# Performance work log

Hardware: AMD Instinct MI355X
Metric: run time of the kernel (lower is better)

## Reference

```python
import jax, jax.numpy as jnp
import numpy as np

B, S, H, NH = 1, 4096, 1024, 16
DH = H // NH


def setup_inputs() -> dict:
    key = jax.random.key(0)
    ks = jax.random.split(key, 9)
    sc = 0.02
    return {
        "queries": jax.random.normal(ks[0], (B, S, H), jnp.float32),
        "keys": jax.random.normal(ks[1], (B, S, H), jnp.float32),
        "values": jax.random.normal(ks[2], (B, S, H), jnp.float32),
        "Wq_w": jax.random.normal(ks[3], (H, H), jnp.float32) * sc,
        "Wq_b": jax.random.normal(ks[4], (H,), jnp.float32) * sc,
        "Wk_w": jax.random.normal(ks[5], (H, H), jnp.float32) * sc,
        "Wk_b": jax.random.normal(ks[6], (H,), jnp.float32) * sc,
        "Wv_w": jax.random.normal(ks[7], (H, H), jnp.float32) * sc,
        "Wv_b": jax.random.normal(ks[8], (H,), jnp.float32) * sc,
    }


def _split_heads(x):
    # torch.chunk(x, NH, dim=-1) then stack(dim=1) == reshape + transpose
    b, s, h = x.shape
    return jnp.transpose(x.reshape(b, s, NH, DH), (0, 2, 1, 3))  # [B,NH,S,DH]


def reference(queries, keys, values, Wq_w, Wq_b, Wk_w, Wk_b, Wv_w, Wv_b):
    q = jax.nn.relu(queries @ Wq_w.T + Wq_b)
    k = jax.nn.relu(keys @ Wk_w.T + Wk_b)
    v = jax.nn.relu(values @ Wv_w.T + Wv_b)
    qh, kh, vh = _split_heads(q), _split_heads(k), _split_heads(v)
    score = jnp.einsum("bhsd,bhtd->bhst", qh, kh) / jnp.sqrt(jnp.float32(DH))
    attn = jax.nn.softmax(score, axis=-1)
    a = jnp.einsum("bhst,bhtd->bhsd", attn, vh)  # [B,NH,S,DH]
    # faithful to torch: permute(0,1,3,2) -> [B,NH,DH,S], then reshape to (B,S,H)
    a = jnp.transpose(a, (0, 1, 3, 2)).reshape(q.shape[0], q.shape[1], q.shape[2])
    return a + queries
```

## Files before the change

kernel.cpp:

```cpp
#include <hip/hip_runtime.h>
#include <stdint.h>


#define SEQ 4096
#define HID 1024
#define NHEAD 16
#define DHEAD 64

typedef __attribute__((ext_vector_type(8))) short short8_t;
typedef __attribute__((ext_vector_type(4))) float f32x4;
typedef __attribute__((ext_vector_type(16))) float f32x16;
typedef __attribute__((ext_vector_type(2))) unsigned int u32x2;

#define WS_QB   0u
#define WS_KB   4194304u
#define WS_VB   8388608u
#define WS_WQ   12582912u
#define WS_QO   15728640u
#define WS_KO   19922944u
#define WS_VT   24117248u

__device__ __forceinline__ unsigned short f2bf(float f) {
  union { float f; unsigned int u; } x; x.f = f;
  unsigned int u = x.u;
  return (unsigned short)((u + 0x7FFFu + ((u >> 16) & 1u)) >> 16);
}

__device__ __forceinline__ float fexp2(float x) {
#if __has_builtin(__builtin_amdgcn_exp2f)
  return __builtin_amdgcn_exp2f(x);
#else
  float r; asm("v_exp_f32 %0, %1" : "=v"(r) : "v"(x)); return r;
#endif
}

__device__ __forceinline__ unsigned int pk2(float a, float b) {
  unsigned int r;
  asm("v_cvt_pk_bf16_f32 %0, %1, %2" : "=v"(r) : "v"(a), "v"(b));
  return r;
}

__device__ __forceinline__ void pl32swap(unsigned int& a, unsigned int& b) {
  asm("v_permlane32_swap_b32 %0, %1" : "+v"(a), "+v"(b));
}

__device__ __forceinline__ void gll16(const void* g, void* l) {
  __builtin_amdgcn_global_load_lds(
      (const __attribute__((address_space(1))) void*)g,
      (__attribute__((address_space(3))) void*)l, 16, 0, 0);
}

__device__ __forceinline__ void packP(const f32x16& a, short8_t& p0,
                                      short8_t& p1) {
  unsigned int w0 = pk2(a[0], a[1]),   w1 = pk2(a[2], a[3]);
  unsigned int w2 = pk2(a[4], a[5]),   w3 = pk2(a[6], a[7]);
  unsigned int w4 = pk2(a[8], a[9]),   w5 = pk2(a[10], a[11]);
  unsigned int w6 = pk2(a[12], a[13]), w7 = pk2(a[14], a[15]);
  pl32swap(w0, w2);
  pl32swap(w1, w3);
  pl32swap(w4, w6);
  pl32swap(w5, w7);
  union { unsigned int u[4]; short8_t v; } q0, q1;
  q0.u[0] = w0; q0.u[1] = w1; q0.u[2] = w2; q0.u[3] = w3;
  q1.u[0] = w4; q1.u[1] = w5; q1.u[2] = w6; q1.u[3] = w7;
  p0 = q0.v; p1 = q1.v;
}

#define MFMA32(a, b, c) __builtin_amdgcn_mfma_f32_32x32x16_bf16(a, b, c, 0, 0, 0)

__global__ void __launch_bounds__(256) prep_convert(
    const float* __restrict__ qin, const float* __restrict__ kin,
    const float* __restrict__ vin, const float* __restrict__ wq,
    const float* __restrict__ wk, const float* __restrict__ wv,
    unsigned short* __restrict__ ws) {
  const int total = 3932160;
  for (int i = blockIdx.x * blockDim.x + threadIdx.x; i < total;
       i += gridDim.x * blockDim.x) {
    const float* src; unsigned short* dst; int off;
    if (i < 3145728) {
      int which = i >> 20;
      off = (i & 1048575) << 2;
      src = which == 0 ? qin : (which == 1 ? kin : vin);
      dst = ws + which * 4194304u;
    } else {
      int j = i - 3145728;
      int which = j >> 18;
      off = (j & 262143) << 2;
      src = which == 0 ? wq : (which == 1 ? wk : wv);
      dst = ws + WS_WQ + which * 1048576u;
    }
    float4 f = *(const float4*)(src + off);
    u32x2 p;
    p.x = f2bf(f.x) | ((unsigned int)f2bf(f.y) << 16);
    p.y = f2bf(f.z) | ((unsigned int)f2bf(f.w) << 16);
    *(u32x2*)(dst + off) = p;
  }
}

__global__ void __launch_bounds__(256) qkv_gemm(
    unsigned short* __restrict__ ws, const float* __restrict__ bq,
    const float* __restrict__ bk, const float* __restrict__ bv) {
  __shared__ alignas(16) unsigned short lA[128 * 32];
  __shared__ alignas(16) unsigned short lB[128 * 32];
  const int z = blockIdx.z;
  const unsigned short* A = ws + z * 4194304u;
  const unsigned short* W = ws + WS_WQ + z * 1048576u;
  const float* bias = z == 0 ? bq : (z == 1 ? bk : bv);
  const int tid = threadIdx.x;
  const int lane = tid & 63;
  const int wid = tid >> 6;
  const int wr = wid >> 1, wc = wid & 1;
  const int lin = blockIdx.y * 8 + blockIdx.x;
  const int nid = (lin & 7) * 32 + (lin >> 3);
  const int bm = nid >> 3, bn = nid & 7;
  const int l15 = lane & 15, l4 = lane >> 4;

  f32x4 acc[4][4];
#pragma unroll
  for (int m = 0; m < 4; ++m)
#pragma unroll
    for (int n = 0; n < 4; ++n) acc[m][n] = {0.f, 0.f, 0.f, 0.f};

  const int srow = lane >> 2;
  const int scs = lane & 3;

  for (int kt = 0; kt < 1024; kt += 32) {
    __syncthreads();
#pragma unroll
    for (int c = 0; c < 2; ++c) {
      const int row = c * 64 + wid * 16 + srow;
      const int ch = scs ^ ((row >> 1) & 3);
      gll16(A + (size_t)(bm * 128 + row) * 1024 + kt + ch * 8,
            (char*)lA + c * 4096 + wid * 1024);
      gll16(W + (size_t)(bn * 128 + row) * 1024 + kt + ch * 8,
            (char*)lB + c * 4096 + wid * 1024);
    }
    __syncthreads();
    short8_t af[4], bf[4];
#pragma unroll
    for (int m = 0; m < 4; ++m) {
      const int row = wr * 64 + m * 16 + l15;
      const int ch = l4 ^ ((row >> 1) & 3);
      af[m] = *(const short8_t*)(lA + row * 32 + ch * 8);
    }
#pragma unroll
    for (int n = 0; n < 4; ++n) {
      const int row = wc * 64 + n * 16 + l15;
      const int ch = l4 ^ ((row >> 1) & 3);
      bf[n] = *(const short8_t*)(lB + row * 32 + ch * 8);
    }
#pragma unroll
    for (int m = 0; m < 4; ++m)
#pragma unroll
      for (int n = 0; n < 4; ++n)
        acc[m][n] = __builtin_amdgcn_mfma_f32_16x16x32_bf16(af[m], bf[n],
                                                            acc[m][n], 0, 0, 0);
  }

  const int row0 = bm * 128 + wr * 64;
  const int col0 = bn * 128 + wc * 64;
  if (z < 2) {
    const float scl = (z == 1) ? 0.18033688011112042f : 1.0f;
    unsigned short* o = ws + WS_QO + z * 4194304u;
#pragma unroll
    for (int n = 0; n < 4; ++n) {
      const int col = col0 + n * 16 + l15;
      const float bb = bias[col];
#pragma unroll
      for (int m = 0; m < 4; ++m)
#pragma unroll
        for (int j = 0; j < 4; ++j) {
          const int row = row0 + m * 16 + l4 * 4 + j;
          o[(size_t)row * 1024 + col] = f2bf(fmaxf(acc[m][n][j] + bb, 0.f) * scl);
        }
    }
  } else {
    unsigned short* vt = ws + WS_VT;
#pragma unroll
    for (int n = 0; n < 4; ++n) {
      const int col = col0 + n * 16 + l15;
      const float bb = bias[col];
      const int nh = col >> 6, d = col & 63;
#pragma unroll
      for (int m = 0; m < 4; ++m) {
        const int t0 = row0 + m * 16 + l4 * 4;
        u32x2 p;
        p.x = f2bf(fmaxf(acc[m][n][0] + bb, 0.f)) |
              ((unsigned int)f2bf(fmaxf(acc[m][n][1] + bb, 0.f)) << 16);
        p.y = f2bf(fmaxf(acc[m][n][2] + bb, 0.f)) |
              ((unsigned int)f2bf(fmaxf(acc[m][n][3] + bb, 0.f)) << 16);
        *(u32x2*)(vt + (size_t)nh * 262144 + (size_t)d * 4096 + t0) = p;
      }
    }
  }
}

__global__ void __launch_bounds__(256, 2) attn_fwd(
    const unsigned short* __restrict__ ws, const float* __restrict__ qin,
    float* __restrict__ out) {
  __shared__ alignas(16) char smem[33792];
  unsigned short* lKb = (unsigned short*)smem;
  unsigned short* lVb = (unsigned short*)(smem + 16384);
  float* fO = (float*)smem;
  float* fRs = (float*)(smem + 33280);

  const unsigned short* qo = ws + WS_QO;
  const char* koB = (const char*)(ws + WS_KO);
  const char* vtB = (const char*)(ws + WS_VT);
  const int nh = blockIdx.y;
  const int qb0 = blockIdx.x * 128;
  const int tid = threadIdx.x, lane = tid & 63, wid = tid >> 6;
  const int l31 = lane & 31, l5 = lane >> 5;
  const int qg = wid >> 1, tw = wid & 1;
  const int sqg = qb0 + qg * 64;

  const int stt = tid >> 3;
  const int sch = tid & 7;
  unsigned kboff[2], vboff[2];
#pragma unroll
  for (int r = 0; r < 2; ++r) {
    const int tt = r * 32 + stt;
    const int ch = sch ^ (tt & 7);
    kboff[r] = (unsigned)(tt * 1024 + nh * 64 + ch * 8) * 2u;
    vboff[r] = (unsigned)(nh * 262144 + tt * 4096 + ch * 8) * 2u;
  }

  short8_t qf[2][4];
#pragma unroll
  for (int cg = 0; cg < 2; ++cg)
#pragma unroll
    for (int kcd = 0; kcd < 4; ++kcd)
      qf[cg][kcd] = *(const short8_t*)(qo + (size_t)(sqg + cg * 32 + l31) * 1024 +
                                       nh * 64 + kcd * 16 + l5 * 8);

  union { unsigned int u[4]; short8_t v; } ou;
  {
    const unsigned int ov = (l31 == 0) ? 0x3F803F80u : 0u;
    ou.u[0] = ov; ou.u[1] = ov; ou.u[2] = ov; ou.u[3] = ov;
  }
  const short8_t ones = ou.v;

  int kofl[4];
  {
    const int row = tw * 32 + l31;
#pragma unroll
    for (int kcd = 0; kcd < 4; ++kcd)
      kofl[kcd] = row * 128 + (((kcd * 2 + l5) ^ (row & 7)) * 16);
  }
  int vofl[2][2];
#pragma unroll
  for (int n = 0; n < 2; ++n) {
    const int row = n * 32 + l31;
#pragma unroll
    for (int kc = 0; kc < 2; ++kc)
      vofl[n][kc] = row * 128 + (((tw * 4 + kc * 2 + l5) ^ (row & 7)) * 16);
  }

  f32x16 zro;
#pragma unroll
  for (int r = 0; r < 16; ++r) zro[r] = 0.f;
  f32x16 aco00 = zro, aco01 = zro, aco10 = zro, aco11 = zro;
  f32x16 acl0 = zro, acl1 = zro;

#define STAGE(buf, kvb)                                                        \
  {                                                                            \
    const unsigned kvbK = (unsigned)(kvb) * 2048u;                             \
    const unsigned kvbV = (unsigned)(kvb) * 2u;                                \
    _Pragma("unroll") for (int r = 0; r < 2; ++r) {                            \
      gll16(koB + (kboff[r] + kvbK),                                           \
            (char*)lKb + (buf) * 8192 + r * 4096 + wid * 1024);                \
      gll16(vtB + (vboff[r] + kvbV),                                           \
            (char*)lVb + (buf) * 8192 + r * 4096 + wid * 1024);                \
    }                                                                          \
  }

  STAGE(0, 0);
  __syncthreads();
  int cur = 0;

  for (int kv = 0; kv < 4096; kv += 64) {
    if (kv + 64 < 4096) STAGE(cur ^ 1, kv + 64);
    const char* lKc = (const char*)lKb + cur * 8192;
    const char* lVc = (const char*)lVb + cur * 8192;

    short8_t kfr[4];
#pragma unroll
    for (int kcd = 0; kcd < 4; ++kcd)
      kfr[kcd] = *(const short8_t*)(lKc + kofl[kcd]);

    __builtin_amdgcn_s_setprio(1);
    f32x16 acs0 = MFMA32(kfr[0], qf[0][0], zro);
    f32x16 acs1 = MFMA32(kfr[0], qf[1][0], zro);
#pragma unroll
    for (int kcd = 1; kcd < 4; ++kcd) {
      acs0 = MFMA32(kfr[kcd], qf[0][kcd], acs0);
      acs1 = MFMA32(kfr[kcd], qf[1][kcd], acs1);
    }
    __builtin_amdgcn_s_setprio(0);

#pragma unroll
    for (int r = 0; r < 16; ++r) {
      acs0[r] = fexp2(acs0[r]);
      acs1[r] = fexp2(acs1[r]);
    }

    short8_t pa00, pa01, pa10, pa11;
    packP(acs0, pa00, pa01);
    packP(acs1, pa10, pa11);

    const short8_t vf00 = *(const short8_t*)(lVc + vofl[0][0]);
    const short8_t vf10 = *(const short8_t*)(lVc + vofl[1][0]);
    const short8_t vf01 = *(const short8_t*)(lVc + vofl[0][1]);
    const short8_t vf11 = *(const short8_t*)(lVc + vofl[1][1]);

    __builtin_amdgcn_s_setprio(1);
    aco00 = MFMA32(pa00, vf00, aco00);
    aco10 = MFMA32(pa10, vf00, aco10);
    aco01 = MFMA32(pa00, vf10, aco01);
    aco11 = MFMA32(pa10, vf10, aco11);
    acl0 = MFMA32(pa00, ones, acl0);
    acl1 = MFMA32(pa10, ones, acl1);
    aco00 = MFMA32(pa01, vf01, aco00);
    aco10 = MFMA32(pa11, vf01, aco10);
    aco01 = MFMA32(pa01, vf11, aco01);
    aco11 = MFMA32(pa11, vf11, aco11);
    acl0 = MFMA32(pa01, ones, acl0);
    acl1 = MFMA32(pa11, ones, acl1);
    __builtin_amdgcn_s_setprio(0);

    __syncthreads();
    cur ^= 1;
  }

#pragma unroll
  for (int p = 0; p < 2; ++p) {
    if (p) __syncthreads();
    if (qg == p) {
      float* myO = fO + tw * 4160;
#pragma unroll
      for (int r = 0; r < 16; ++r) {
        const int sl = (r & 3) + 8 * (r >> 2) + 4 * l5;
        myO[l31 * 65 + sl] = aco00[r];
        myO[(l31 + 32) * 65 + sl] = aco01[r];
        myO[l31 * 65 + 32 + sl] = aco10[r];
        myO[(l31 + 32) * 65 + 32 + sl] = aco11[r];
      }
      if (l31 == 0) {
#pragma unroll
        for (int r = 0; r < 16; ++r) {
          const int sl = (r & 3) + 8 * (r >> 2) + 4 * l5;
          fRs[tw * 64 + sl] = acl0[r];
          fRs[tw * 64 + 32 + sl] = acl1[r];
        }
      }
    }
    __syncthreads();
    {
      const int s = tid & 63;
      const int sg = qb0 + p * 64 + s;
      const float inv = 1.f / (fRs[s] + fRs[64 + s]);
      const int scol = sg & 1023, srow = sg >> 10;
#pragma unroll
      for (int i = 0; i < 16; ++i) {
        const int d = (tid >> 6) * 16 + i;
        const float v = fO[d * 65 + s] + fO[4160 + d * 65 + s];
        const int idx = (nh * 256 + d * 4 + srow) * 1024 + scol;
        out[idx] = qin[idx] + v * inv;
      }
    }
  }
#undef STAGE
}

extern "C" void kernel_launch(void* const* d_in, const int* in_sizes, int n_in,
                              void* d_out, int out_size, void* d_ws,
                              size_t ws_size, hipStream_t stream) {
  const float* qin = (const float*)d_in[0];
  const float* kin = (const float*)d_in[1];
  const float* vin = (const float*)d_in[2];
  const float* wq = (const float*)d_in[3];
  const float* bq = (const float*)d_in[4];
  const float* wk = (const float*)d_in[5];
  const float* bk = (const float*)d_in[6];
  const float* wv = (const float*)d_in[7];
  const float* bv = (const float*)d_in[8];
  unsigned short* ws = (unsigned short*)d_ws;
  float* out = (float*)d_out;

  prep_convert<<<dim3(8192), dim3(256), 0, stream>>>(qin, kin, vin, wq, wk, wv, ws);
  qkv_gemm<<<dim3(8, 32, 3), dim3(256), 0, stream>>>(ws, bq, bk, bv);
  attn_fwd<<<dim3(32, 16), dim3(256), 0, stream>>>(ws, qin, out);
}
```

Baseline: 136.6 us.

## Software-pipeline attention loop: compute next QK^T while doing exp and PV of current tile

Splits K and V staging into separate macros. K is now prefetched two tiles ahead and V one tile ahead. The QK^T MFMAs for the next KV tile are issued before the exp, pack and PV MFMAs of the current tile, with a peeled epilogue for the last tile. The aim is to hide exp/VALU latency and LDS reads behind matrix-core work. In exchange it keeps an extra pair of 16-float score accumulators live, which raises register pressure and may lower occupancy.

```diff
diff --git a/kernel.cpp b/kernel.cpp
--- a/kernel.cpp
+++ b/kernel.cpp
@@ -262,40 +262,48 @@
   f32x16 aco00 = zro, aco01 = zro, aco10 = zro, aco11 = zro;
   f32x16 acl0 = zro, acl1 = zro;
 
-#define STAGE(buf, kvb)                                                        \
+#define STAGEK(buf, kvb)                                                       \
   {                                                                            \
-    const unsigned kvbK = (unsigned)(kvb) * 2048u;                             \
-    const unsigned kvbV = (unsigned)(kvb) * 2u;                                \
-    _Pragma("unroll") for (int r = 0; r < 2; ++r) {                            \
-      gll16(koB + (kboff[r] + kvbK),                                           \
-            (char*)lKb + (buf) * 8192 + r * 4096 + wid * 1024);                \
-      gll16(vtB + (vboff[r] + kvbV),                                           \
-            (char*)lVb + (buf) * 8192 + r * 4096 + wid * 1024);                \
+    const unsigned kk_ = (unsigned)(kvb) * 2048u;                              \
+    _Pragma("unroll") for (int r = 0; r < 2; ++r)                              \
+        gll16(koB + (kboff[r] + kk_),                                          \
+              (char*)lKb + (buf) * 8192 + r * 4096 + wid * 1024);              \
+  }
+#define STAGEV(buf, kvb)                                                       \
+  {                                                                            \
+    const unsigned vv_ = (unsigned)(kvb) * 2u;                                 \
+    _Pragma("unroll") for (int r = 0; r < 2; ++r)                              \
+        gll16(vtB + (vboff[r] + vv_),                                          \
+              (char*)lVb + (buf) * 8192 + r * 4096 + wid * 1024);              \
+  }
+#define QKT(kb, a0, a1)                                                        \
+  {                                                                            \
+    const char* lKc_ = (const char*)lKb + (kb) * 8192;                         \
+    short8_t kfr_[4];                                                          \
+    _Pragma("unroll") for (int kcd = 0; kcd < 4; ++kcd)                        \
+        kfr_[kcd] = *(const short8_t*)(lKc_ + kofl[kcd]);                      \
+    a0 = MFMA32(kfr_[0], qf[0][0], zro);                                       \
+    a1 = MFMA32(kfr_[0], qf[1][0], zro);                                       \
+    _Pragma("unroll") for (int kcd = 1; kcd < 4; ++kcd) {                      \
+      a0 = MFMA32(kfr_[kcd], qf[0][kcd], a0);                                  \
+      a1 = MFMA32(kfr_[kcd], qf[1][kcd], a1);                                  \
     }                                                                          \
   }
 
-  STAGE(0, 0);
+  STAGEK(0, 0);
+  STAGEV(0, 0);
+  STAGEK(1, 64);
   __syncthreads();
-  int cur = 0;
-
-  for (int kv = 0; kv < 4096; kv += 64) {
-    if (kv + 64 < 4096) STAGE(cur ^ 1, kv + 64);
-    const char* lKc = (const char*)lKb + cur * 8192;
-    const char* lVc = (const char*)lVb + cur * 8192;
-
-    short8_t kfr[4];
-#pragma unroll
-    for (int kcd = 0; kcd < 4; ++kcd)
-      kfr[kcd] = *(const short8_t*)(lKc + kofl[kcd]);
-
+  f32x16 acs0, acs1;
+  QKT(0, acs0, acs1);
+
+  for (int i = 0; i < 63; ++i) {
+    if (i < 62) STAGEK(i & 1, (i + 2) << 6);
+    STAGEV((i + 1) & 1, (i + 1) << 6);
+
+    f32x16 acsN0, acsN1;
     __builtin_amdgcn_s_setprio(1);
-    f32x16 acs0 = MFMA32(kfr[0], qf[0][0], zro);
-    f32x16 acs1 = MFMA32(kfr[0], qf[1][0], zro);
-#pragma unroll
-    for (int kcd = 1; kcd < 4; ++kcd) {
-      acs0 = MFMA32(kfr[kcd], qf[0][kcd], acs0);
-      acs1 = MFMA32(kfr[kcd], qf[1][kcd], acs1);
-    }
+    QKT((i + 1) & 1, acsN0, acsN1);
     __builtin_amdgcn_s_setprio(0);
 
 #pragma unroll
@@ -303,16 +311,15 @@
       acs0[r] = fexp2(acs0[r]);
       acs1[r] = fexp2(acs1[r]);
     }
-
     short8_t pa00, pa01, pa10, pa11;
     packP(acs0, pa00, pa01);
     packP(acs1, pa10, pa11);
 
+    const char* lVc = (const char*)lVb + (i & 1) * 8192;
     const short8_t vf00 = *(const short8_t*)(lVc + vofl[0][0]);
     const short8_t vf10 = *(const short8_t*)(lVc + vofl[1][0]);
     const short8_t vf01 = *(const short8_t*)(lVc + vofl[0][1]);
     const short8_t vf11 = *(const short8_t*)(lVc + vofl[1][1]);
-
     __builtin_amdgcn_s_setprio(1);
     aco00 = MFMA32(pa00, vf00, aco00);
     aco10 = MFMA32(pa10, vf00, aco10);
@@ -329,8 +336,38 @@
     __builtin_amdgcn_s_setprio(0);
 
     __syncthreads();
-    cur ^= 1;
-  }
+    acs0 = acsN0;
+    acs1 = acsN1;
+  }
+
+  {
+#pragma unroll
+    for (int r = 0; r < 16; ++r) {
+      acs0[r] = fexp2(acs0[r]);
+      acs1[r] = fexp2(acs1[r]);
+    }
+    short8_t pa00, pa01, pa10, pa11;
+    packP(acs0, pa00, pa01);
+    packP(acs1, pa10, pa11);
+    const char* lVc = (const char*)lVb + 8192;
+    const short8_t vf00 = *(const short8_t*)(lVc + vofl[0][0]);
+    const short8_t vf10 = *(const short8_t*)(lVc + vofl[1][0]);
+    const short8_t vf01 = *(const short8_t*)(lVc + vofl[0][1]);
+    const short8_t vf11 = *(const short8_t*)(lVc + vofl[1][1]);
+    aco00 = MFMA32(pa00, vf00, aco00);
+    aco10 = MFMA32(pa10, vf00, aco10);
+    aco01 = MFMA32(pa00, vf10, aco01);
+    aco11 = MFMA32(pa10, vf10, aco11);
+    acl0 = MFMA32(pa00, ones, acl0);
+    acl1 = MFMA32(pa10, ones, acl1);
+    aco00 = MFMA32(pa01, vf01, aco00);
+    aco10 = MFMA32(pa11, vf01, aco10);
+    aco01 = MFMA32(pa01, vf11, aco01);
+    aco11 = MFMA32(pa11, vf11, aco11);
+    acl0 = MFMA32(pa01, ones, acl0);
+    acl1 = MFMA32(pa11, ones, acl1);
+  }
+  __syncthreads();
 
 #pragma unroll
   for (int p = 0; p < 2; ++p) {
@@ -369,7 +406,9 @@
       }
     }
   }
-#undef STAGE
+#undef STAGEK
+#undef STAGEV
+#undef QKT
 }
 
 extern "C" void kernel_launch(void* const* d_in, const int* in_sizes, int n_in,
```

Result: no change. 137.9 us (+0.9%).

## Triple-buffer GEMM and attention loads, widen attention blocks, compute row sums in VALU

Applied to the files above, without the earlier changes.

The QKV GEMM moves from a single LDS buffer with two barriers per k-step to a three-slot ring. Loads are issued two iterations ahead and gated by vmcnt waits with one barrier per step. The attention kernel now runs 512 threads over 256 queries per block, sharing each K/V tile among eight waves, with a three-slot K/V ring of the same kind. The softmax denominator is accumulated with VALU adds and a lane shuffle instead of extra MFMAs against a ones vector. This cuts per-iteration synchronisation and MFMA work and halves K/V reloads. The cost is more LDS, higher register pressure and a four-pass serialized epilogue.

```diff
diff --git a/kernel.cpp b/kernel.cpp
--- a/kernel.cpp
+++ b/kernel.cpp
@@ -100,8 +100,8 @@
 __global__ void __launch_bounds__(256) qkv_gemm(
     unsigned short* __restrict__ ws, const float* __restrict__ bq,
     const float* __restrict__ bk, const float* __restrict__ bv) {
-  __shared__ alignas(16) unsigned short lA[128 * 32];
-  __shared__ alignas(16) unsigned short lB[128 * 32];
+  __shared__ alignas(16) unsigned short lA[3][128 * 32];
+  __shared__ alignas(16) unsigned short lB[3][128 * 32];
   const int z = blockIdx.z;
   const unsigned short* A = ws + z * 4194304u;
   const unsigned short* W = ws + WS_WQ + z * 1048576u;
@@ -124,30 +124,45 @@
   const int srow = lane >> 2;
   const int scs = lane & 3;
 
-  for (int kt = 0; kt < 1024; kt += 32) {
-    __syncthreads();
-#pragma unroll
-    for (int c = 0; c < 2; ++c) {
-      const int row = c * 64 + wid * 16 + srow;
-      const int ch = scs ^ ((row >> 1) & 3);
-      gll16(A + (size_t)(bm * 128 + row) * 1024 + kt + ch * 8,
-            (char*)lA + c * 4096 + wid * 1024);
-      gll16(W + (size_t)(bn * 128 + row) * 1024 + kt + ch * 8,
-            (char*)lB + c * 4096 + wid * 1024);
-    }
-    __syncthreads();
+#define GSTAGE(slot, it)                                                       \
+  {                                                                            \
+    const int kt_ = (it) * 32;                                                 \
+    _Pragma("unroll") for (int c = 0; c < 2; ++c) {                            \
+      const int row = c * 64 + wid * 16 + srow;                                \
+      const int ch = scs ^ ((row >> 1) & 3);                                   \
+      gll16(A + (size_t)(bm * 128 + row) * 1024 + kt_ + ch * 8,                \
+            (char*)lA + (slot) * 8192 + c * 4096 + wid * 1024);                \
+      gll16(W + (size_t)(bn * 128 + row) * 1024 + kt_ + ch * 8,                \
+            (char*)lB + (slot) * 8192 + c * 4096 + wid * 1024);                \
+    }                                                                          \
+  }
+
+  GSTAGE(0, 0);
+  GSTAGE(1, 1);
+
+  for (int it = 0; it < 32; ++it) {
+    asm volatile("s_waitcnt vmcnt(4)" ::: "memory");
+    __builtin_amdgcn_s_barrier();
+    __builtin_amdgcn_sched_barrier(0);
+    {
+      const int tn = (it + 2 < 32) ? it + 2 : 31;
+      const int sl = (it + 2) % 3;
+      GSTAGE(sl, tn);
+    }
+    const unsigned short* sA = lA[0] + (it % 3) * 4096;
+    const unsigned short* sB = lB[0] + (it % 3) * 4096;
     short8_t af[4], bf[4];
 #pragma unroll
     for (int m = 0; m < 4; ++m) {
       const int row = wr * 64 + m * 16 + l15;
       const int ch = l4 ^ ((row >> 1) & 3);
-      af[m] = *(const short8_t*)(lA + row * 32 + ch * 8);
+      af[m] = *(const short8_t*)(sA + row * 32 + ch * 8);
     }
 #pragma unroll
     for (int n = 0; n < 4; ++n) {
       const int row = wc * 64 + n * 16 + l15;
       const int ch = l4 ^ ((row >> 1) & 3);
-      bf[n] = *(const short8_t*)(lB + row * 32 + ch * 8);
+      bf[n] = *(const short8_t*)(sB + row * 32 + ch * 8);
     }
 #pragma unroll
     for (int m = 0; m < 4; ++m)
@@ -156,6 +171,7 @@
         acc[m][n] = __builtin_amdgcn_mfma_f32_16x16x32_bf16(af[m], bf[n],
                                                             acc[m][n], 0, 0, 0);
   }
+#undef GSTAGE
 
   const int row0 = bm * 128 + wr * 64;
   const int col0 = bn * 128 + wc * 64;
@@ -195,12 +211,10 @@
   }
 }
 
-__global__ void __launch_bounds__(256, 2) attn_fwd(
+__global__ void __launch_bounds__(512, 2) attn_fwd(
     const unsigned short* __restrict__ ws, const float* __restrict__ qin,
     float* __restrict__ out) {
-  __shared__ alignas(16) char smem[33792];
-  unsigned short* lKb = (unsigned short*)smem;
-  unsigned short* lVb = (unsigned short*)(smem + 16384);
+  __shared__ alignas(16) char smem[49152];
   float* fO = (float*)smem;
   float* fRs = (float*)(smem + 33280);
 
@@ -208,37 +222,27 @@
   const char* koB = (const char*)(ws + WS_KO);
   const char* vtB = (const char*)(ws + WS_VT);
   const int nh = blockIdx.y;
-  const int qb0 = blockIdx.x * 128;
+  const int qb0 = blockIdx.x * 256;
   const int tid = threadIdx.x, lane = tid & 63, wid = tid >> 6;
   const int l31 = lane & 31, l5 = lane >> 5;
   const int qg = wid >> 1, tw = wid & 1;
-  const int sqg = qb0 + qg * 64;
 
   const int stt = tid >> 3;
   const int sch = tid & 7;
-  unsigned kboff[2], vboff[2];
-#pragma unroll
-  for (int r = 0; r < 2; ++r) {
-    const int tt = r * 32 + stt;
-    const int ch = sch ^ (tt & 7);
-    kboff[r] = (unsigned)(tt * 1024 + nh * 64 + ch * 8) * 2u;
-    vboff[r] = (unsigned)(nh * 262144 + tt * 4096 + ch * 8) * 2u;
-  }
+  const unsigned kgoff =
+      (unsigned)(stt * 1024 + nh * 64 + ((sch ^ (stt & 7)) * 8)) * 2u;
+  const unsigned vgoff =
+      (unsigned)(nh * 262144 + stt * 4096 + ((sch ^ (stt & 7)) * 8)) * 2u;
+  const unsigned ldst = (unsigned)tid * 16u;
 
   short8_t qf[2][4];
 #pragma unroll
-  for (int cg = 0; cg < 2; ++cg)
+  for (int c = 0; c < 2; ++c)
 #pragma unroll
     for (int kcd = 0; kcd < 4; ++kcd)
-      qf[cg][kcd] = *(const short8_t*)(qo + (size_t)(sqg + cg * 32 + l31) * 1024 +
-                                       nh * 64 + kcd * 16 + l5 * 8);
-
-  union { unsigned int u[4]; short8_t v; } ou;
-  {
-    const unsigned int ov = (l31 == 0) ? 0x3F803F80u : 0u;
-    ou.u[0] = ov; ou.u[1] = ov; ou.u[2] = ov; ou.u[3] = ov;
-  }
-  const short8_t ones = ou.v;
+      qf[c][kcd] = *(const short8_t*)(
+          qo + (size_t)(qb0 + qg * 64 + c * 32 + l31) * 1024 + nh * 64 +
+          kcd * 16 + l5 * 8);
 
   int kofl[4];
   {
@@ -260,33 +264,36 @@
 #pragma unroll
   for (int r = 0; r < 16; ++r) zro[r] = 0.f;
   f32x16 aco00 = zro, aco01 = zro, aco10 = zro, aco11 = zro;
-  f32x16 acl0 = zro, acl1 = zro;
-
-#define STAGE(buf, kvb)                                                        \
+  float rsa0 = 0.f, rsa1 = 0.f, rsa2 = 0.f, rsa3 = 0.f;
+  float rsb0 = 0.f, rsb1 = 0.f, rsb2 = 0.f, rsb3 = 0.f;
+
+#define STAGE(slot, ti)                                                        \
   {                                                                            \
-    const unsigned kvbK = (unsigned)(kvb) * 2048u;                             \
-    const unsigned kvbV = (unsigned)(kvb) * 2u;                                \
-    _Pragma("unroll") for (int r = 0; r < 2; ++r) {                            \
-      gll16(koB + (kboff[r] + kvbK),                                           \
-            (char*)lKb + (buf) * 8192 + r * 4096 + wid * 1024);                \
-      gll16(vtB + (vboff[r] + kvbV),                                           \
-            (char*)lVb + (buf) * 8192 + r * 4096 + wid * 1024);                \
-    }                                                                          \
+    gll16(koB + (kgoff + (unsigned)(ti) * 131072u),                            \
+          smem + (slot) * 16384 + ldst);                                       \
+    gll16(vtB + (vgoff + (unsigned)(ti) * 128u),                               \
+          smem + (slot) * 16384 + 8192 + ldst);                                \
   }
 
   STAGE(0, 0);
-  __syncthreads();
-  int cur = 0;
-
-  for (int kv = 0; kv < 4096; kv += 64) {
-    if (kv + 64 < 4096) STAGE(cur ^ 1, kv + 64);
-    const char* lKc = (const char*)lKb + cur * 8192;
-    const char* lVc = (const char*)lVb + cur * 8192;
+  STAGE(1, 1);
+  asm volatile("s_waitcnt vmcnt(4)" ::: "memory");
+
+  for (int i = 0; i < 64; ++i) {
+    asm volatile("s_waitcnt vmcnt(2)" ::: "memory");
+    __builtin_amdgcn_s_barrier();
+    __builtin_amdgcn_sched_barrier(0);
+    {
+      const int tn = (i + 2 < 64) ? i + 2 : 63;
+      STAGE((i + 2) % 3, tn);
+    }
+    const char* sK = smem + (i % 3) * 16384;
+    const char* sV = sK + 8192;
 
     short8_t kfr[4];
 #pragma unroll
     for (int kcd = 0; kcd < 4; ++kcd)
-      kfr[kcd] = *(const short8_t*)(lKc + kofl[kcd]);
+      kfr[kcd] = *(const short8_t*)(sK + kofl[kcd]);
 
     __builtin_amdgcn_s_setprio(1);
     f32x16 acs0 = MFMA32(kfr[0], qf[0][0], zro);
@@ -299,42 +306,54 @@
     __builtin_amdgcn_s_setprio(0);
 
 #pragma unroll
-    for (int r = 0; r < 16; ++r) {
-      acs0[r] = fexp2(acs0[r]);
-      acs1[r] = fexp2(acs1[r]);
+    for (int r = 0; r < 16; r += 4) {
+      const float a0 = fexp2(acs0[r]),     a1 = fexp2(acs0[r + 1]);
+      const float a2 = fexp2(acs0[r + 2]), a3 = fexp2(acs0[r + 3]);
+      acs0[r] = a0; acs0[r + 1] = a1; acs0[r + 2] = a2; acs0[r + 3] = a3;
+      rsa0 += a0; rsa1 += a1; rsa2 += a2; rsa3 += a3;
+      const float b0 = fexp2(acs1[r]),     b1 = fexp2(acs1[r + 1]);
+      const float b2 = fexp2(acs1[r + 2]), b3 = fexp2(acs1[r + 3]);
+      acs1[r] = b0; acs1[r + 1] = b1; acs1[r + 2] = b2; acs1[r + 3] = b3;
+      rsb0 += b0; rsb1 += b1; rsb2 += b2; rsb3 += b3;
     }
 
     short8_t pa00, pa01, pa10, pa11;
     packP(acs0, pa00, pa01);
     packP(acs1, pa10, pa11);
 
-    const short8_t vf00 = *(const short8_t*)(lVc + vofl[0][0]);
-    const short8_t vf10 = *(const short8_t*)(lVc + vofl[1][0]);
-    const short8_t vf01 = *(const short8_t*)(lVc + vofl[0][1]);
-    const short8_t vf11 = *(const short8_t*)(lVc + vofl[1][1]);
+    const short8_t vf00 = *(const short8_t*)(sV + vofl[0][0]);
+    const short8_t vf10 = *(const short8_t*)(sV + vofl[1][0]);
+    const short8_t vf01 = *(const short8_t*)(sV + vofl[0][1]);
+    const short8_t vf11 = *(const short8_t*)(sV + vofl[1][1]);
 
     __builtin_amdgcn_s_setprio(1);
     aco00 = MFMA32(pa00, vf00, aco00);
     aco10 = MFMA32(pa10, vf00, aco10);
     aco01 = MFMA32(pa00, vf10, aco01);
     aco11 = MFMA32(pa10, vf10, aco11);
-    acl0 = MFMA32(pa00, ones, acl0);
-    acl1 = MFMA32(pa10, ones, acl1);
     aco00 = MFMA32(pa01, vf01, aco00);
     aco10 = MFMA32(pa11, vf01, aco10);
     aco01 = MFMA32(pa01, vf11, aco01);
     aco11 = MFMA32(pa11, vf11, aco11);
-    acl0 = MFMA32(pa01, ones, acl0);
-    acl1 = MFMA32(pa11, ones, acl1);
     __builtin_amdgcn_s_setprio(0);
-
-    __syncthreads();
-    cur ^= 1;
-  }
-
-#pragma unroll
-  for (int p = 0; p < 2; ++p) {
-    if (p) __syncthreads();
+  }
+#undef STAGE
+
+  float rsA = (rsa0 + rsa1) + (rsa2 + rsa3);
+  float rsB = (rsb0 + rsb1) + (rsb2 + rsb3);
+  rsA += __shfl_xor(rsA, 32);
+  rsB += __shfl_xor(rsB, 32);
+
+  asm volatile("s_waitcnt vmcnt(0)" ::: "memory");
+  __builtin_amdgcn_s_barrier();
+
+  if (l5 == 0) {
+    fRs[tw * 256 + qg * 64 + l31] = rsA;
+    fRs[tw * 256 + qg * 64 + 32 + l31] = rsB;
+  }
+
+#pragma unroll 1
+  for (int p = 0; p < 4; ++p) {
     if (qg == p) {
       float* myO = fO + tw * 4160;
 #pragma unroll
@@ -345,31 +364,24 @@
         myO[l31 * 65 + 32 + sl] = aco10[r];
         myO[(l31 + 32) * 65 + 32 + sl] = aco11[r];
       }
-      if (l31 == 0) {
-#pragma unroll
-        for (int r = 0; r < 16; ++r) {
-          const int sl = (r & 3) + 8 * (r >> 2) + 4 * l5;
-          fRs[tw * 64 + sl] = acl0[r];
-          fRs[tw * 64 + 32 + sl] = acl1[r];
-        }
-      }
     }
     __syncthreads();
     {
       const int s = tid & 63;
+      const int dg = tid >> 6;
       const int sg = qb0 + p * 64 + s;
-      const float inv = 1.f / (fRs[s] + fRs[64 + s]);
+      const float inv = 1.f / (fRs[p * 64 + s] + fRs[256 + p * 64 + s]);
       const int scol = sg & 1023, srow = sg >> 10;
 #pragma unroll
-      for (int i = 0; i < 16; ++i) {
-        const int d = (tid >> 6) * 16 + i;
+      for (int i = 0; i < 8; ++i) {
+        const int d = dg * 8 + i;
         const float v = fO[d * 65 + s] + fO[4160 + d * 65 + s];
         const int idx = (nh * 256 + d * 4 + srow) * 1024 + scol;
         out[idx] = qin[idx] + v * inv;
       }
     }
-  }
-#undef STAGE
+    __syncthreads();
+  }
 }
 
 extern "C" void kernel_launch(void* const* d_in, const int* in_sizes, int n_in,
@@ -389,5 +401,5 @@
 
   prep_convert<<<dim3(8192), dim3(256), 0, stream>>>(qin, kin, vin, wq, wk, wv, ws);
   qkv_gemm<<<dim3(8, 32, 3), dim3(256), 0, stream>>>(ws, bq, bk, bv);
-  attn_fwd<<<dim3(32, 16), dim3(256), 0, stream>>>(ws, qin, out);
-}
+  attn_fwd<<<dim3(16, 16), dim3(512), 0, stream>>>(ws, qin, out);
+}
```

New measurement: 146.9 us. 7.5% more time.
